# Performance work log

Hardware: AMD Instinct MI355X
Metric: run time of the kernel (lower is better)

## Reference

```python
import jax, jax.numpy as jnp
import numpy as np

C, H, W = 8, 8, 8
A = 6            # action_dim
LATENT = 64
HID = 64
GRU_IN = HID + A + LATENT  # 134


def _conv(x, w):
    return jax.lax.conv_general_dilated(
        x, w, (1, 1), 'VALID', dimension_numbers=('NCHW', 'OIHW', 'NCHW'))


def setup_inputs() -> dict:
    key = jax.random.key(0)
    ks = jax.random.split(key, 20)
    B, N, T = 64, 10, 128
    s_h = jax.random.normal(ks[0], (B, N, T, C, H, W), jnp.float32)
    a_h = jax.random.randint(ks[1], (B, N, T), 0, A).astype(jnp.int64)
    b_z = jax.random.normal(ks[2], (B, LATENT), jnp.float32)
    s = 0.05
    p = {
        'conv1_w': jax.random.normal(ks[3], (32, C, 3, 3)) * s,
        'conv1_b': jnp.zeros((32,)),
        'conv2_w': jax.random.normal(ks[4], (32, 32, 3, 3)) * s,
        'conv2_b': jnp.zeros((32,)),
        'fc_w': jax.random.normal(ks[5], (HID, 32 * 4 * 4)) * s,
        'fc_b': jnp.zeros((HID,)),
        'emb': jax.random.normal(ks[6], (A, A)) * s,
        'gru_wih': jax.random.normal(ks[7], (3 * HID, GRU_IN)) * s,
        'gru_whh': jax.random.normal(ks[8], (3 * HID, HID)) * s,
        'gru_bih': jnp.zeros((3 * HID,)),
        'gru_bhh': jnp.zeros((3 * HID,)),
        'mlp1_w': jax.random.normal(ks[9], (HID, HID)) * s,
        'mlp1_b': jnp.zeros((HID,)),
        'mlp2_w': jax.random.normal(ks[10], (A, HID)) * s,
        'mlp2_b': jnp.zeros((A,)),
    }
    return {'s_h': s_h, 'a_h': a_h, 'b_z': b_z, **p}


def reference(s_h, a_h, b_z, conv1_w, conv1_b, conv2_w, conv2_b, fc_w, fc_b,
              emb, gru_wih, gru_whh, gru_bih, gru_bhh,
              mlp1_w, mlp1_b, mlp2_w, mlp2_b):
    B, N = s_h.shape[0], s_h.shape[1]
    T = a_h.shape[2]
    BN = B * N

    # action mask, [B, N, T, 1]
    action_masks = (a_h != A - 1)[..., None].astype(jnp.float32)

    # --- state encoder on first frame only ---
    s0 = s_h[:, :, 0].reshape(BN, C, H, W)
    x = jax.nn.relu(_conv(s0, conv1_w) + conv1_b[:, None, None])
    x = jax.nn.relu(_conv(x, conv2_w) + conv2_b[:, None, None])
    x = x.reshape(BN, -1)                       # [BN, 512]
    state_emb = jax.nn.relu(x @ fc_w.T + fc_b)  # [BN, HID]

    bz = jnp.broadcast_to(b_z[:, None, :], (B, N, LATENT)).reshape(BN, LATENT)

    h0 = jnp.zeros((BN, HID), s_h.dtype)
    act0 = jnp.full((BN,), A - 1, jnp.int32)

    def step(carry, _):
        h, act = carry
        a_emb = emb[act]                                          # [BN, A]
        inp = jnp.concatenate([state_emb, a_emb, bz], axis=-1)    # [BN, GRU_IN]
        gx = inp @ gru_wih.T + gru_bih
        gh = h @ gru_whh.T + gru_bhh
        xr, xz, xn = jnp.split(gx, 3, axis=-1)
        hr, hz, hn = jnp.split(gh, 3, axis=-1)
        r = jax.nn.sigmoid(xr + hr)
        z = jax.nn.sigmoid(xz + hz)
        n = jnp.tanh(xn + r * hn)
        h_new = (1.0 - z) * n + z * h
        hid = jnp.tanh(h_new @ mlp1_w.T + mlp1_b)
        logits = hid @ mlp2_w.T + mlp2_b                          # [BN, A]
        next_act = jax.lax.stop_gradient(jnp.argmax(logits, axis=-1)).astype(jnp.int32)
        return (h_new, next_act), logits

    (_, _), logits_seq = jax.lax.scan(step, (h0, act0), None, length=T - 1)
    # logits_seq: [T-1, BN, A] -> [B, N, T-1, A]
    logits_all = jnp.transpose(logits_seq, (1, 0, 2)).reshape(B, N, T - 1, A)
    return logits_all, action_masks
```

## Files before the change

### kernel.cpp

```cpp
#include <hip/hip_runtime.h>

#define A_DIM 6
#define HID_D 64
#define LATENT_D 64
#define GRU_IN_D 134
#define T_STEPS 128
#define N_ENV 10
#define BN_TOT 640

typedef float f2 __attribute__((ext_vector_type(2)));

__device__ __forceinline__ float fast_sigmoid(float x) {
    return __builtin_amdgcn_rcpf(1.0f + __builtin_amdgcn_exp2f(-1.4426950408889634f * x));
}
__device__ __forceinline__ float fast_tanh(float x) {
    return 1.0f - 2.0f * __builtin_amdgcn_rcpf(1.0f + __builtin_amdgcn_exp2f(2.8853900817779268f * x));
}

template<int CTRL>
__device__ __forceinline__ float dppadd(float v) {
    int t = __builtin_amdgcn_update_dpp(0, __builtin_bit_cast(int, v), CTRL, 0xf, 0xf, true);
    return v + __builtin_bit_cast(float, t);
}
__device__ __forceinline__ float wave_reduce_add(float v) {
    v = dppadd<0x111>(v);
    v = dppadd<0x112>(v);
    v = dppadd<0x114>(v);
    v = dppadd<0x118>(v);
    v = dppadd<0x142>(v);
    v = dppadd<0x143>(v);
    return __builtin_bit_cast(float, __builtin_amdgcn_readlane(__builtin_bit_cast(int, v), 63));
}

__global__ __launch_bounds__(128, 1)
void policy_kernel(const float* __restrict__ s_h,
                   const int*   __restrict__ a_h,
                   const float* __restrict__ b_z,
                   const float* __restrict__ conv1_w, const float* __restrict__ conv1_b,
                   const float* __restrict__ conv2_w, const float* __restrict__ conv2_b,
                   const float* __restrict__ fc_w,    const float* __restrict__ fc_b,
                   const float* __restrict__ emb,
                   const float* __restrict__ gru_wih, const float* __restrict__ gru_whh,
                   const float* __restrict__ gru_bih, const float* __restrict__ gru_bhh,
                   const float* __restrict__ mlp1_w,  const float* __restrict__ mlp1_b,
                   const float* __restrict__ mlp2_w,  const float* __restrict__ mlp2_b,
                   float* __restrict__ logits_out, float* __restrict__ mask_out)
{
    __shared__ __align__(16) float s0[512];
    __shared__ __align__(16) float a1[1152];
    __shared__ __align__(16) float a2[512];
    __shared__ __align__(16) float pfc[128];
    __shared__ __align__(16) float semb[64];
    __shared__ __align__(16) float gxc[192];
    __shared__ __align__(16) float atab[6*192];
    __shared__ __align__(16) float hbuf[64];
    __shared__ __align__(16) f2   partA[128];
    __shared__ __align__(16) f2   partB[128];

    const int bn  = blockIdx.x;
    const int tid = threadIdx.x;
    const int j   = tid & 63;
    const int w   = tid >> 6;

    mask_out[bn * T_STEPS + tid] = (a_h[bn * T_STEPS + tid] != (A_DIM - 1)) ? 1.0f : 0.0f;

    {
        const float* src = s_h + (size_t)bn * T_STEPS * 512;
        #pragma unroll
        for (int i = 0; i < 4; ++i) s0[tid + i * 128] = src[tid + i * 128];
    }
    __syncthreads();

    for (int i = tid; i < 1152; i += 128) {
        const int oc = i / 36, r = i % 36, oh = r / 6, ow = r % 6;
        float sum = conv1_b[oc];
        const float* wp = conv1_w + oc * 72;
        #pragma unroll
        for (int ic = 0; ic < 8; ++ic)
            #pragma unroll
            for (int kh = 0; kh < 3; ++kh)
                #pragma unroll
                for (int kw = 0; kw < 3; ++kw)
                    sum = fmaf(s0[ic * 64 + (oh + kh) * 8 + (ow + kw)],
                               wp[ic * 9 + kh * 3 + kw], sum);
        a1[i] = fmaxf(sum, 0.0f);
    }
    __syncthreads();

    for (int i = tid; i < 512; i += 128) {
        const int oc = i / 16, r = i % 16, oh = r / 4, ow = r % 4;
        float sum = conv2_b[oc];
        const float* wp = conv2_w + oc * 288;
        for (int ic = 0; ic < 32; ++ic)
            #pragma unroll
            for (int kh = 0; kh < 3; ++kh)
                #pragma unroll
                for (int kw = 0; kw < 3; ++kw)
                    sum = fmaf(a1[ic * 36 + (oh + kh) * 6 + (ow + kw)],
                               wp[ic * 9 + kh * 3 + kw], sum);
        a2[i] = fmaxf(sum, 0.0f);
    }
    __syncthreads();

    {
        const int o = j, hf = w;
        const float* wp = fc_w + o * 512 + hf * 256;
        const float* ap = a2 + hf * 256;
        float s0a = 0.f, s1a = 0.f, s2a = 0.f, s3a = 0.f;
        for (int k = 0; k < 256; k += 4) {
            s0a = fmaf(ap[k + 0], wp[k + 0], s0a);
            s1a = fmaf(ap[k + 1], wp[k + 1], s1a);
            s2a = fmaf(ap[k + 2], wp[k + 2], s2a);
            s3a = fmaf(ap[k + 3], wp[k + 3], s3a);
        }
        pfc[tid] = (s0a + s1a) + (s2a + s3a);
    }
    __syncthreads();
    if (tid < 64) semb[tid] = fmaxf(pfc[tid] + pfc[tid + 64] + fc_b[tid], 0.0f);
    __syncthreads();

    {
        const float* bz = b_z + (size_t)(bn / N_ENV) * LATENT_D;
        for (int g = tid; g < 192; g += 128) {
            float sum = gru_bih[g] + ((g < 128) ? gru_bhh[g] : 0.0f);
            const float* wp = gru_wih + g * GRU_IN_D;
            for (int k = 0; k < 64; ++k) sum = fmaf(semb[k], wp[k], sum);
            for (int k = 0; k < 64; ++k) sum = fmaf(bz[k], wp[70 + k], sum);
            gxc[g] = sum;
        }
    }
    for (int i = tid; i < 6 * 192; i += 128) {
        const int a = i / 192, g = i % 192;
        float sum = 0.0f;
        #pragma unroll
        for (int q = 0; q < 6; ++q)
            sum = fmaf(emb[a * 6 + q], gru_wih[g * GRU_IN_D + 64 + q], sum);
        atab[i] = sum;
    }
    __syncthreads();

    f2 wr[16], wz[16], wn[16], w1[16];
    {
        const float* pr = gru_whh + (size_t)j * 64 + 32 * w;
        const float* pz = gru_whh + (size_t)(64 + j) * 64 + 32 * w;
        const float* pn = gru_whh + (size_t)(128 + j) * 64 + 32 * w;
        const float* p1 = mlp1_w + (size_t)j * 64 + 32 * w;
        #pragma unroll
        for (int i = 0; i < 8; ++i) {
            float4 v;
            v = ((const float4*)pr)[i]; wr[2*i] = (f2){v.x, v.y}; wr[2*i+1] = (f2){v.z, v.w};
            v = ((const float4*)pz)[i]; wz[2*i] = (f2){v.x, v.y}; wz[2*i+1] = (f2){v.z, v.w};
            v = ((const float4*)pn)[i]; wn[2*i] = (f2){v.x, v.y}; wn[2*i+1] = (f2){v.z, v.w};
            v = ((const float4*)p1)[i]; w1[2*i] = (f2){v.x, v.y}; w1[2*i+1] = (f2){v.z, v.w};
        }
    }
    const float gxr = gxc[j], gxz = gxc[64 + j], gxn = gxc[128 + j];
    const float bhn = gru_bhh[128 + j];
    const float b1j = mlp1_b[j];
    float ar[6], az[6], an[6], m2c[6], b2[6];
    #pragma unroll
    for (int a = 0; a < 6; ++a) {
        ar[a] = atab[a * 192 + j];
        az[a] = atab[a * 192 + 64 + j];
        an[a] = atab[a * 192 + 128 + j];
        m2c[a] = mlp2_w[a * 64 + j];
        b2[a] = mlp2_b[a];
    }

    float hprev = 0.0f;
    float hr_c = 0.0f, hz_c = 0.0f, hn_c = bhn;
    int act = A_DIM - 1;
    float* lout = logits_out + (size_t)bn * (T_STEPS - 1) * A_DIM;
    const float4* hv4 = (const float4*)hbuf + w * 8;

    for (int t = 0; t < T_STEPS - 1; ++t) {
        float sr = ar[0], sz = az[0], sn = an[0];
        #pragma unroll
        for (int a = 1; a < 6; ++a) {
            const bool c = (act == a);
            sr = c ? ar[a] : sr; sz = c ? az[a] : sz; sn = c ? an[a] : sn;
        }
        const float r = fast_sigmoid(gxr + sr + hr_c);
        const float z = fast_sigmoid(gxz + sz + hz_c);
        const float n = fast_tanh(fmaf(r, hn_c, gxn + sn));
        const float hnew = fmaf(z, hprev - n, n);
        hprev = hnew;

        if (w == 0) hbuf[j] = hnew;
        __syncthreads();

        f2 pr = {0.f, 0.f}, pz = {0.f, 0.f}, pn = {0.f, 0.f}, p1 = {0.f, 0.f};
        #pragma unroll
        for (int i = 0; i < 8; ++i) {
            const float4 hv = hv4[i];
            const f2 ha = (f2){hv.x, hv.y};
            const f2 hb = (f2){hv.z, hv.w};
            pr += ha * wr[2*i]; pr += hb * wr[2*i+1];
            pz += ha * wz[2*i]; pz += hb * wz[2*i+1];
            pn += ha * wn[2*i]; pn += hb * wn[2*i+1];
            p1 += ha * w1[2*i]; p1 += hb * w1[2*i+1];
        }
        const float mr = pr.x + pr.y, mz = pz.x + pz.y;
        const float mn = pn.x + pn.y, m1 = p1.x + p1.y;
        partA[(w << 6) | j] = (f2){mr, mz};
        partB[(w << 6) | j] = (f2){mn, m1};
        __syncthreads();
        const f2 oA = partA[((1 - w) << 6) | j];
        const f2 oB = partB[((1 - w) << 6) | j];
        hr_c = mr + oA.x;
        hz_c = mz + oA.y;
        hn_c = mn + oB.x + bhn;
        const float h1f = m1 + oB.y + b1j;

        const float hid = fast_tanh(h1f);

        const float l0 = wave_reduce_add(hid * m2c[0]) + b2[0];
        const float l1 = wave_reduce_add(hid * m2c[1]) + b2[1];
        const float l2 = wave_reduce_add(hid * m2c[2]) + b2[2];
        const float l3 = wave_reduce_add(hid * m2c[3]) + b2[3];
        const float l4 = wave_reduce_add(hid * m2c[4]) + b2[4];
        const float l5 = wave_reduce_add(hid * m2c[5]) + b2[5];

        float best = l0; int bi = 0;
        if (l1 > best) { best = l1; bi = 1; }
        if (l2 > best) { best = l2; bi = 2; }
        if (l3 > best) { best = l3; bi = 3; }
        if (l4 > best) { best = l4; bi = 4; }
        if (l5 > best) { best = l5; bi = 5; }
        act = bi;

        if (tid < A_DIM) {
            const float outv = (j == 0) ? l0 : (j == 1) ? l1 : (j == 2) ? l2
                             : (j == 3) ? l3 : (j == 4) ? l4 : l5;
            lout[t * A_DIM + j] = outv;
        }
    }
}

extern "C" void kernel_launch(void* const* d_in, const int* in_sizes, int n_in,
                              void* d_out, int out_size, void* d_ws, size_t ws_size,
                              hipStream_t stream) {
    const float* s_h     = (const float*)d_in[0];
    const int*   a_h     = (const int*)  d_in[1];
    const float* b_z     = (const float*)d_in[2];
    const float* conv1_w = (const float*)d_in[3];
    const float* conv1_b = (const float*)d_in[4];
    const float* conv2_w = (const float*)d_in[5];
    const float* conv2_b = (const float*)d_in[6];
    const float* fc_w    = (const float*)d_in[7];
    const float* fc_b    = (const float*)d_in[8];
    const float* emb     = (const float*)d_in[9];
    const float* gru_wih = (const float*)d_in[10];
    const float* gru_whh = (const float*)d_in[11];
    const float* gru_bih = (const float*)d_in[12];
    const float* gru_bhh = (const float*)d_in[13];
    const float* mlp1_w  = (const float*)d_in[14];
    const float* mlp1_b  = (const float*)d_in[15];
    const float* mlp2_w  = (const float*)d_in[16];
    const float* mlp2_b  = (const float*)d_in[17];

    float* out = (float*)d_out;
    float* logits_out = out;
    float* mask_out   = out + (size_t)BN_TOT * (T_STEPS - 1) * A_DIM;

    policy_kernel<<<BN_TOT, 128, 0, stream>>>(
        s_h, a_h, b_z, conv1_w, conv1_b, conv2_w, conv2_b, fc_w, fc_b, emb,
        gru_wih, gru_whh, gru_bih, gru_bhh, mlp1_w, mlp1_b, mlp2_w, mlp2_b,
        logits_out, mask_out);
}
```

Before: 523.9 us.

## Replace per-step block barrier with wave-private h buffer and double-buffered exchange

Each wave now writes its own copy of the new hidden state into a private shared buffer under wave barriers instead of wave 0 writing a shared buffer followed by a block-wide __syncthreads. The two partial-sum exchange arrays are merged into one float4 exchange that is double-buffered on t parity, so each timestep needs only one block barrier instead of two. The aim is to cut barrier latency in the serial 127-step GRU recurrence, at the cost of relying on both waves computing identical hnew values and on the parity buffering being safe against the next iteration's writes.

```diff
diff --git a/kernel.cpp b/kernel.cpp
--- a/kernel.cpp
+++ b/kernel.cpp
@@ -53,9 +53,8 @@
     __shared__ __align__(16) float semb[64];
     __shared__ __align__(16) float gxc[192];
     __shared__ __align__(16) float atab[6*192];
-    __shared__ __align__(16) float hbuf[64];
-    __shared__ __align__(16) f2   partA[128];
-    __shared__ __align__(16) f2   partB[128];
+    __shared__ __align__(16) float hpriv[2][64];
+    __shared__ __align__(16) float4 pex[2][2][64];
 
     const int bn  = blockIdx.x;
     const int tid = threadIdx.x;
@@ -103,9 +102,8 @@
     __syncthreads();
 
     {
-        const int o = j, hf = w;
-        const float* wp = fc_w + o * 512 + hf * 256;
-        const float* ap = a2 + hf * 256;
+        const float* wp = fc_w + j * 512 + w * 256;
+        const float* ap = a2 + w * 256;
         float s0a = 0.f, s1a = 0.f, s2a = 0.f, s3a = 0.f;
         for (int k = 0; k < 256; k += 4) {
             s0a = fmaf(ap[k + 0], wp[k + 0], s0a);
@@ -171,7 +169,7 @@
     float hr_c = 0.0f, hz_c = 0.0f, hn_c = bhn;
     int act = A_DIM - 1;
     float* lout = logits_out + (size_t)bn * (T_STEPS - 1) * A_DIM;
-    const float4* hv4 = (const float4*)hbuf + w * 8;
+    const float4* hp4 = (const float4*)(&hpriv[w][0]) + w * 8;
 
     for (int t = 0; t < T_STEPS - 1; ++t) {
         float sr = ar[0], sz = az[0], sn = an[0];
@@ -186,13 +184,14 @@
         const float hnew = fmaf(z, hprev - n, n);
         hprev = hnew;
 
-        if (w == 0) hbuf[j] = hnew;
-        __syncthreads();
+        __builtin_amdgcn_wave_barrier();
+        hpriv[w][j] = hnew;
+        __builtin_amdgcn_wave_barrier();
 
         f2 pr = {0.f, 0.f}, pz = {0.f, 0.f}, pn = {0.f, 0.f}, p1 = {0.f, 0.f};
         #pragma unroll
         for (int i = 0; i < 8; ++i) {
-            const float4 hv = hv4[i];
+            const float4 hv = hp4[i];
             const f2 ha = (f2){hv.x, hv.y};
             const f2 hb = (f2){hv.z, hv.w};
             pr += ha * wr[2*i]; pr += hb * wr[2*i+1];
@@ -202,17 +201,14 @@
         }
         const float mr = pr.x + pr.y, mz = pz.x + pz.y;
         const float mn = pn.x + pn.y, m1 = p1.x + p1.y;
-        partA[(w << 6) | j] = (f2){mr, mz};
-        partB[(w << 6) | j] = (f2){mn, m1};
+
+        pex[t & 1][w][j] = (float4){mr, mz, mn, m1};
         __syncthreads();
-        const f2 oA = partA[((1 - w) << 6) | j];
-        const f2 oB = partB[((1 - w) << 6) | j];
-        hr_c = mr + oA.x;
-        hz_c = mz + oA.y;
-        hn_c = mn + oB.x + bhn;
-        const float h1f = m1 + oB.y + b1j;
-
-        const float hid = fast_tanh(h1f);
+        const float4 o = pex[t & 1][w ^ 1][j];
+        hr_c = mr + o.x;
+        hz_c = mz + o.y;
+        hn_c = mn + o.z + bhn;
+        const float hid = fast_tanh(m1 + o.w + b1j);
 
         const float l0 = wave_reduce_add(hid * m2c[0]) + b2[0];
         const float l1 = wave_reduce_add(hid * m2c[1]) + b2[1];
```

After: 517.0 us. Within noise of the previous version (-1.3%).
